# Kernel tuning notes

Hardware: AMD Instinct MI355X
Metric: run time of the kernel (lower is better)

## Reference

```python
import jax, jax.numpy as jnp
import numpy as np

_J6 = jnp.array([[0,0,0,0,0,1],[0,0,0,0,-1,0],[0,0,0,1,0,0],
                 [0,0,1,0,0,0],[0,-1,0,0,0,0],[1,0,0,0,0,0]], dtype=jnp.float32)
_PAIRS4 = [(0,1),(0,2),(0,3),(1,2),(1,3),(2,3)]
H = 16  # n_heads

def _ln(x, g, b, eps=1e-5):
    m = jnp.mean(x, axis=-1, keepdims=True)
    v = jnp.var(x, axis=-1, keepdims=True)
    return (x - m) / jnp.sqrt(v + eps) * g + b

def _exterior(p1, p2):
    # Plucker coordinates of the line through p1,p2 in R^4 -> R^6, normalized
    parts = [p1[..., i] * p2[..., j] - p1[..., j] * p2[..., i] for i, j in _PAIRS4]
    L = jnp.stack(parts, axis=-1)
    n = jnp.linalg.norm(L, axis=-1, keepdims=True)
    return L / jnp.maximum(n, 1e-12)

def _iterated_gram_attn(x, Wqkv, bqkv, W1w, W2w, W1r, W2r, Wmv, bmv, Wmg, bmg,
                        mem_scale, iter_mix, decay_logits, Wout, bout):
    B, T, D = x.shape
    dh = D // H
    # ---- standard causal attention branch ----
    qkv = (x @ Wqkv + bqkv).reshape(B, T, 3, H, dh)
    q = jnp.transpose(qkv[:, :, 0], (0, 2, 1, 3))  # bhtd
    k = jnp.transpose(qkv[:, :, 1], (0, 2, 1, 3))
    v = jnp.transpose(qkv[:, :, 2], (0, 2, 1, 3))
    scores = jnp.einsum('bhtd,bhsd->bhts', q, k) * (dh ** -0.5)
    causal = jnp.tril(jnp.ones((T, T), dtype=bool))
    scores = jnp.where(causal, scores, -jnp.inf)
    attn = jax.nn.softmax(scores, axis=-1)  # dropout is eval-mode identity
    seq_out = jnp.einsum('bhts,bhsd->bhtd', attn, v).transpose(0, 2, 1, 3).reshape(B, T, D)
    # ---- Gram memory branch ----
    x_prev = jnp.concatenate([jnp.zeros_like(x[:, :1]), x[:, :-1]], axis=1)
    w1 = (x_prev @ W1w).reshape(B, T, H, 4)
    w2 = (x @ W2w).reshape(B, T, H, 4)
    write_lines = _exterior(w1, w2)                       # (B,T,H,6)
    r1 = (x @ W1r).reshape(B, T, H, 4)
    r2 = (x @ W2r).reshape(B, T, H, 4)
    read_lines = _exterior(r1, r2)                        # (B,T,H,6)
    Jw = jnp.einsum('bthi,ij->bhtj', write_lines, _J6)    # (B,H,T,6)
    rd = jnp.transpose(read_lines, (0, 2, 1, 3))          # (B,H,T,6)
    decays = jax.nn.sigmoid(decay_logits)                 # (H,)
    pos = jnp.arange(T, dtype=x.dtype)
    outer = Jw[..., :, None] * Jw[..., None, :]           # (B,H,T,6,6)
    dinv = (1.0 / jnp.maximum(decays, 1e-6))[:, None] ** pos[None, :]  # (H,T)
    M = jnp.cumsum(outer * dinv[None, :, :, None, None], axis=2)
    M = jnp.concatenate([jnp.zeros_like(M[:, :, :1]), M[:, :, :-1]], axis=2)  # shift: strictly past
    dfwd = decays[:, None] ** pos[None, :]
    M = M * dfwd[None, :, :, None, None]                  # (B,H,T,6,6)
    rdM = jnp.einsum('bhti,bhtij->bhtj', rd, M)
    score_M = jnp.sum(rdM * rd, axis=-1)                  # (B,H,T)
    score_M2 = jnp.sum(rdM * rdM, axis=-1)
    alpha = jax.nn.sigmoid(iter_mix[0])
    mem_score = (1 - alpha) * score_M + alpha * score_M2
    mem_val = x @ Wmv + bmv                               # (B,T,D)
    gate = jax.nn.sigmoid(x @ Wmg + bmg)                  # (B,T,H)
    gated = jax.nn.sigmoid(jnp.transpose(mem_score, (0, 2, 1)) * mem_scale[None, None, :]) * gate
    gated = jnp.mean(gated, axis=-1, keepdims=True)       # (B,T,1)
    return (seq_out + gated * mem_val) @ Wout + bout

def _block(x, ln1_g, ln1_b, Wqkv, bqkv, W1w, W2w, W1r, W2r, Wmv, bmv, Wmg, bmg,
           mem_scale, iter_mix, decay_logits, Wout, bout,
           ln2_g, ln2_b, Wfc, bfc, Wproj, bproj):
    h = _ln(x, ln1_g, ln1_b)
    x = x + _iterated_gram_attn(h, Wqkv, bqkv, W1w, W2w, W1r, W2r, Wmv, bmv,
                                Wmg, bmg, mem_scale, iter_mix, decay_logits, Wout, bout)
    h2 = _ln(x, ln2_g, ln2_b)
    mlp = jax.nn.gelu(h2 @ Wfc + bfc, approximate=False) @ Wproj + bproj
    return x + mlp

def setup_inputs() -> dict:
    key = jax.random.key(0)
    B, T, D = 2, 1024, 1024
    dff = 4 * D
    ks = jax.random.split(key, 16)
    s = 0.02
    inp = {
        'x': jax.random.normal(ks[0], (B, T, D), jnp.float32),
        'ln1_g': jnp.ones((D,), jnp.float32), 'ln1_b': jnp.zeros((D,), jnp.float32),
        'Wqkv': jax.random.normal(ks[1], (D, 3 * D), jnp.float32) * s,
        'bqkv': jnp.zeros((3 * D,), jnp.float32),
        'W1w': jax.random.normal(ks[2], (D, 4 * H), jnp.float32) * s,
        'W2w': jax.random.normal(ks[3], (D, 4 * H), jnp.float32) * s,
        'W1r': jax.random.normal(ks[4], (D, 4 * H), jnp.float32) * s,
        'W2r': jax.random.normal(ks[5], (D, 4 * H), jnp.float32) * s,
        'Wmv': jax.random.normal(ks[6], (D, D), jnp.float32) * s,
        'bmv': jnp.zeros((D,), jnp.float32),
        'Wmg': jax.random.normal(ks[7], (D, H), jnp.float32) * s,
        'bmg': jnp.zeros((H,), jnp.float32),
        'mem_scale': jnp.full((H,), 0.1, jnp.float32),
        'iter_mix': jnp.zeros((1,), jnp.float32),
        'decay_logits': jnp.full((H,), 4.6, jnp.float32) + 0.1 * jax.random.normal(ks[8], (H,), jnp.float32),
        'Wout': jax.random.normal(ks[9], (D, D), jnp.float32) * s,
        'bout': jnp.zeros((D,), jnp.float32),
        'ln2_g': jnp.ones((D,), jnp.float32), 'ln2_b': jnp.zeros((D,), jnp.float32),
        'Wfc': jax.random.normal(ks[10], (D, dff), jnp.float32) * s,
        'bfc': jnp.zeros((dff,), jnp.float32),
        'Wproj': jax.random.normal(ks[11], (dff, D), jnp.float32) * s,
        'bproj': jnp.zeros((D,), jnp.float32),
    }
    return inp

def reference(x, ln1_g, ln1_b, Wqkv, bqkv, W1w, W2w, W1r, W2r, Wmv, bmv, Wmg, bmg,
              mem_scale, iter_mix, decay_logits, Wout, bout,
              ln2_g, ln2_b, Wfc, bfc, Wproj, bproj):
    return _block(x, ln1_g, ln1_b, Wqkv, bqkv, W1w, W2w, W1r, W2r, Wmv, bmv, Wmg, bmg,
                  mem_scale, iter_mix, decay_logits, Wout, bout,
                  ln2_g, ln2_b, Wfc, bfc, Wproj, bproj)
```

## Files before the change

### kernel.cpp

```cpp
#include <hip/hip_runtime.h>
#include <hip/hip_bf16.h>
#include <math.h>

typedef float f32x4 __attribute__((ext_vector_type(4)));
typedef _Float16 f16x8 __attribute__((ext_vector_type(8)));
typedef _Float16 f16x4 __attribute__((ext_vector_type(4)));

#define TT 1024
#define DD 1024
#define QS 4608

typedef __attribute__((address_space(1))) const void gas_void;
typedef __attribute__((address_space(3))) void las_void;
static __device__ __forceinline__ void gl_lds16(const void* g, void* l) {
  __builtin_amdgcn_global_load_lds((gas_void*)g, (las_void*)l, 16, 0, 0);
}

__global__ __launch_bounds__(256) void gemm_t16(
    const _Float16* __restrict__ A, const _Float16* __restrict__ Wt,
    const float* __restrict__ bias, void* __restrict__ Cv,
    int N, int K, int act, int gx, int mode, int ktiles) {
  __shared__ __align__(16) _Float16 As[2][128 * 32];
  __shared__ __align__(16) _Float16 Bs[2][128 * 32];
  const int tid = threadIdx.x;
  const int lane = tid & 63;
  const int wid = tid >> 6;
  const int wr = wid >> 1, wc = wid & 1;
  const int g = lane >> 4, l16 = lane & 15;
  const int cpx = gridDim.x >> 3;
  const int wg = (blockIdx.x & 7) * cpx + (blockIdx.x >> 3);
  const int row0 = (wg / gx) * 128, col0 = (wg % gx) * 128;
  const int kbeg = blockIdx.y * ktiles * 32;

  f32x4 acc[4][4];
#pragma unroll
  for (int m = 0; m < 4; ++m)
#pragma unroll
    for (int n = 0; n < 4; ++n) acc[m][n] = (f32x4){0.f, 0.f, 0.f, 0.f};

  const int srow = tid >> 2;
  const int goff = ((tid & 3) ^ ((srow >> 1) & 3)) << 3;
  const _Float16* agp = A + (size_t)(row0 + srow) * K + goff;
  const _Float16* bgp = Wt + (size_t)(col0 + srow) * K + goff;
  const size_t half = (size_t)64 * K;
  const int ldst = wid * 64 * 16;

  const int prm = (l16 >> 1) & 3;

#pragma unroll
  for (int i = 0; i < 2; ++i) {
    gl_lds16(agp + i * half + kbeg, (char*)As[0] + i * 4096 + ldst);
    gl_lds16(bgp + i * half + kbeg, (char*)Bs[0] + i * 4096 + ldst);
  }
  __syncthreads();

  int cur = 0;
  for (int kt = 0; kt < ktiles; ++kt) {
    if (kt + 1 < ktiles) {
      const int kp = kbeg + (kt + 1) * 32;
#pragma unroll
      for (int i = 0; i < 2; ++i) {
        gl_lds16(agp + i * half + kp, (char*)As[cur ^ 1] + i * 4096 + ldst);
        gl_lds16(bgp + i * half + kp, (char*)Bs[cur ^ 1] + i * 4096 + ldst);
      }
    }
    f16x8 af[4], bf[4];
#pragma unroll
    for (int m = 0; m < 4; ++m) {
      const int r = wr * 64 + m * 16 + l16;
      af[m] = *(const f16x8*)(As[cur] + r * 32 + ((g ^ prm) << 3));
    }
#pragma unroll
    for (int n = 0; n < 4; ++n) {
      const int r = wc * 64 + n * 16 + l16;
      bf[n] = *(const f16x8*)(Bs[cur] + r * 32 + ((g ^ prm) << 3));
    }
#pragma unroll
    for (int m = 0; m < 4; ++m)
#pragma unroll
      for (int n = 0; n < 4; ++n)
        acc[m][n] = __builtin_amdgcn_mfma_f32_16x16x32_f16(af[m], bf[n], acc[m][n], 0, 0, 0);
    __syncthreads();
    cur ^= 1;
  }
#pragma unroll
  for (int m = 0; m < 4; ++m) {
#pragma unroll
    for (int n = 0; n < 4; ++n) {
      const int col = col0 + wc * 64 + n * 16 + l16;
      const float bv = (mode != 2 && bias) ? bias[col] : 0.f;
#pragma unroll
      for (int rg = 0; rg < 4; ++rg) {
        const int row = row0 + wr * 64 + m * 16 + g * 4 + rg;
        const size_t off = (size_t)row * N + col;
        float v = acc[m][n][rg] + bv;
        if (act == 1) v = 0.5f * v * (1.f + erff(v * 0.70710678118654752f));
        if (mode == 2) atomicAdd(&((float*)Cv)[off], v);
        else ((_Float16*)Cv)[off] = (_Float16)v;
      }
    }
  }
}

__global__ __launch_bounds__(256) void transT(const float* __restrict__ W,
                                              _Float16* __restrict__ WT, int K, int N) {
  __shared__ float tile[64][65];
  const int n0 = blockIdx.x * 64, k0 = blockIdx.y * 64;
  const int tn = threadIdx.x & 63, tk4 = threadIdx.x >> 6;
#pragma unroll
  for (int it = 0; it < 16; ++it) {
    const int k = k0 + it * 4 + tk4;
    tile[tn][it * 4 + tk4] = W[(size_t)k * N + n0 + tn];
  }
  __syncthreads();
  const int on = threadIdx.x >> 2, ok = threadIdx.x & 3;
  f16x8 a, b;
#pragma unroll
  for (int j = 0; j < 8; ++j) {
    a[j] = (_Float16)tile[on][ok * 16 + j];
    b[j] = (_Float16)tile[on][ok * 16 + 8 + j];
  }
  _Float16* dst = WT + (size_t)(n0 + on) * K + k0 + ok * 16;
  *(f16x8*)dst = a;
  *(f16x8*)(dst + 8) = b;
}

__global__ __launch_bounds__(256) void prep_megaT(
    const float* __restrict__ Wqkv, const float* __restrict__ W1w, const float* __restrict__ W2w,
    const float* __restrict__ W1r, const float* __restrict__ W2r, const float* __restrict__ Wmg,
    const float* __restrict__ Wmv, _Float16* __restrict__ WmT) {
  __shared__ float tile[64][65];
  const int n0 = blockIdx.x * 64, k0 = blockIdx.y * 64;
  const int tn = threadIdx.x & 63, tk4 = threadIdx.x >> 6;
#pragma unroll
  for (int it = 0; it < 16; ++it) {
    const int k = k0 + it * 4 + tk4;
    const int n = n0 + tn;
    float v;
    if (n < 3072) v = Wqkv[(size_t)k * 3072 + n];
    else if (n < 3136) v = W1w[k * 64 + n - 3072];
    else if (n < 3200) v = W2w[k * 64 + n - 3136];
    else if (n < 3264) v = W1r[k * 64 + n - 3200];
    else if (n < 3328) v = W2r[k * 64 + n - 3264];
    else if (n < 3344) v = Wmg[k * 16 + n - 3328];
    else if (n < 3584) v = 0.f;
    else v = Wmv[(size_t)k * 1024 + n - 3584];
    tile[tn][it * 4 + tk4] = v;
  }
  __syncthreads();
  const int on = threadIdx.x >> 2, ok = threadIdx.x & 3;
  f16x8 a, b;
#pragma unroll
  for (int j = 0; j < 8; ++j) {
    a[j] = (_Float16)tile[on][ok * 16 + j];
    b[j] = (_Float16)tile[on][ok * 16 + 8 + j];
  }
  _Float16* dst = WmT + (size_t)(n0 + on) * 1024 + k0 + ok * 16;
  *(f16x8*)dst = a;
  *(f16x8*)(dst + 8) = b;
}

__global__ void bm_init(const float* __restrict__ bqkv, const float* __restrict__ bmg,
                        const float* __restrict__ bmv, float* __restrict__ bm) {
  const int col = blockIdx.x * 256 + threadIdx.x;
  if (col >= 4608) return;
  float b = 0.f;
  if (col < 3072) b = bqkv[col];
  else if (col >= 3328 && col < 3344) b = bmg[col - 3328];
  else if (col >= 3584) b = bmv[col - 3584];
  bm[col] = b;
}

__global__ __launch_bounds__(256) void ln16(const float* __restrict__ in,
    const float* __restrict__ gw, const float* __restrict__ bw, _Float16* __restrict__ out) {
  const int row = blockIdx.x, tid = threadIdx.x;
  const float* x = in + (size_t)row * DD;
  const float4 v = *(const float4*)(x + tid * 4);
  float s = v.x + v.y + v.z + v.w;
  float sq = v.x * v.x + v.y * v.y + v.z * v.z + v.w * v.w;
#pragma unroll
  for (int off = 32; off >= 1; off >>= 1) { s += __shfl_xor(s, off); sq += __shfl_xor(sq, off); }
  __shared__ float red[8];
  const int lane = tid & 63, wv = tid >> 6;
  if (lane == 0) { red[wv] = s; red[4 + wv] = sq; }
  __syncthreads();
  s = red[0] + red[1] + red[2] + red[3];
  sq = red[4] + red[5] + red[6] + red[7];
  const float mean = s * (1.f / 1024.f);
  const float var = sq * (1.f / 1024.f) - mean * mean;
  const float rstd = rsqrtf(var + 1e-5f);
  const float4 g4 = *(const float4*)(gw + tid * 4);
  const float4 b4 = *(const float4*)(bw + tid * 4);
  f16x4 o;
  o[0] = (_Float16)((v.x - mean) * rstd * g4.x + b4.x);
  o[1] = (_Float16)((v.y - mean) * rstd * g4.y + b4.y);
  o[2] = (_Float16)((v.z - mean) * rstd * g4.z + b4.z);
  o[3] = (_Float16)((v.w - mean) * rstd * g4.w + b4.w);
  *(f16x4*)(out + (size_t)row * DD + tid * 4) = o;
}

static __device__ __forceinline__ int swzA(int row, int k) {
  return row * 64 + ((((k >> 3) ^ row) & 7) << 3) + (k & 7);
}
static __device__ __forceinline__ int swzV(int row, int k) {
  return row * 64 + ((((k >> 3) ^ row ^ (row >> 3)) & 7) << 3) + (k & 7);
}

__global__ __launch_bounds__(256) void attn_mfma(const _Float16* __restrict__ qkv,
                                                 _Float16* __restrict__ seq_out) {
  __shared__ __align__(16) _Float16 Kl[64 * 64];
  __shared__ __align__(16) _Float16 Vt[64 * 64];
  __shared__ __align__(16) _Float16 Pl[4][16 * 64];
  const int tid = threadIdx.x, lane = tid & 63, wq = tid >> 6;
  const int g = lane >> 4, l16 = lane & 15;
  const int qt = blockIdx.x, hh = blockIdx.y, bb = blockIdx.z;
  const int nt = qt + 1;

  f16x8 qf[2];
  {
    const _Float16* qp = qkv + (size_t)(bb * TT + qt * 64 + wq * 16 + l16) * QS + hh * 64;
#pragma unroll
    for (int ks = 0; ks < 2; ++ks) {
      const f16x8 a = *(const f16x8*)(qp + ks * 32 + g * 8);
#pragma unroll
      for (int j = 0; j < 8; ++j) qf[ks][j] = (_Float16)((float)a[j] * 0.125f);
    }
  }

  f32x4 oacc[4];
#pragma unroll
  for (int n = 0; n < 4; ++n) oacc[n] = (f32x4){0.f, 0.f, 0.f, 0.f};
  float m[4] = {-INFINITY, -INFINITY, -INFINITY, -INFINITY};
  float l[4] = {0.f, 0.f, 0.f, 0.f};

  const int skey = tid >> 2, sc4 = tid & 3;

  for (int tt = 0; tt < nt; ++tt) {
    if (tt) __syncthreads();
    {
      const _Float16* kp = qkv + (size_t)(bb * TT + tt * 64 + skey) * QS + hh * 64 + 1024;
      const _Float16* vp = kp + 1024;
#pragma unroll
      for (int ii = 0; ii < 4; ++ii) {
        const int d0 = sc4 * 4 + ii * 16;
        *(f16x4*)(Kl + swzA(skey, d0)) = *(const f16x4*)(kp + d0);
        const f16x4 vv = *(const f16x4*)(vp + d0);
        Vt[swzV(d0 + 0, skey)] = vv[0];
        Vt[swzV(d0 + 1, skey)] = vv[1];
        Vt[swzV(d0 + 2, skey)] = vv[2];
        Vt[swzV(d0 + 3, skey)] = vv[3];
      }
    }
    __syncthreads();
    f32x4 s[4];
#pragma unroll
    for (int n = 0; n < 4; ++n) s[n] = (f32x4){0.f, 0.f, 0.f, 0.f};
#pragma unroll
    for (int ks = 0; ks < 2; ++ks) {
      f16x8 kf[4];
#pragma unroll
      for (int n = 0; n < 4; ++n) kf[n] = *(const f16x8*)(Kl + swzA(n * 16 + l16, ks * 32 + g * 8));
#pragma unroll
      for (int n = 0; n < 4; ++n)
        s[n] = __builtin_amdgcn_mfma_f32_16x16x32_f16(qf[ks], kf[n], s[n], 0, 0, 0);
    }
    if (tt == qt) {
      const int rloc = wq * 16 + g * 4;
#pragma unroll
      for (int n = 0; n < 4; ++n) {
        const int cloc = n * 16 + l16;
#pragma unroll
        for (int reg = 0; reg < 4; ++reg)
          if (cloc > rloc + reg) s[n][reg] = -INFINITY;
      }
    }
    float f[4];
#pragma unroll
    for (int reg = 0; reg < 4; ++reg) {
      float t = fmaxf(fmaxf(s[0][reg], s[1][reg]), fmaxf(s[2][reg], s[3][reg]));
#pragma unroll
      for (int off = 1; off < 16; off <<= 1) t = fmaxf(t, __shfl_xor(t, off));
      const float nm = fmaxf(m[reg], t);
      f[reg] = __expf(m[reg] - nm);
      m[reg] = nm;
    }
    float rs[4] = {0.f, 0.f, 0.f, 0.f};
#pragma unroll
    for (int n = 0; n < 4; ++n) {
#pragma unroll
      for (int reg = 0; reg < 4; ++reg) {
        const float p = __expf(s[n][reg] - m[reg]);
        rs[reg] += p;
        Pl[wq][swzA(g * 4 + reg, n * 16 + l16)] = (_Float16)p;
      }
    }
#pragma unroll
    for (int reg = 0; reg < 4; ++reg) {
      float t = rs[reg];
#pragma unroll
      for (int off = 1; off < 16; off <<= 1) t += __shfl_xor(t, off);
      l[reg] = l[reg] * f[reg] + t;
    }
#pragma unroll
    for (int n = 0; n < 4; ++n)
#pragma unroll
      for (int reg = 0; reg < 4; ++reg) oacc[n][reg] *= f[reg];
#pragma unroll
    for (int ks = 0; ks < 2; ++ks) {
      const f16x8 pa = *(const f16x8*)(Pl[wq] + swzA(l16, ks * 32 + g * 8));
      f16x8 vb[4];
#pragma unroll
      for (int n = 0; n < 4; ++n) vb[n] = *(const f16x8*)(Vt + swzV(n * 16 + l16, ks * 32 + g * 8));
#pragma unroll
      for (int n = 0; n < 4; ++n)
        oacc[n] = __builtin_amdgcn_mfma_f32_16x16x32_f16(pa, vb[n], oacc[n], 0, 0, 0);
    }
  }
#pragma unroll
  for (int n = 0; n < 4; ++n) {
#pragma unroll
    for (int reg = 0; reg < 4; ++reg) {
      const int r = qt * 64 + wq * 16 + g * 4 + reg;
      seq_out[(size_t)(bb * TT + r) * DD + hh * 64 + n * 16 + l16] = (_Float16)(oacc[n][reg] / l[reg]);
    }
  }
}

static __device__ __forceinline__ void ext6(const float* a, const float* b, float* L) {
  L[0] = a[0] * b[1] - a[1] * b[0];
  L[1] = a[0] * b[2] - a[2] * b[0];
  L[2] = a[0] * b[3] - a[3] * b[0];
  L[3] = a[1] * b[2] - a[2] * b[1];
  L[4] = a[1] * b[3] - a[3] * b[1];
  L[5] = a[2] * b[3] - a[3] * b[2];
  const float n = sqrtf(L[0]*L[0] + L[1]*L[1] + L[2]*L[2] + L[3]*L[3] + L[4]*L[4] + L[5]*L[5]);
  const float s = 1.f / fmaxf(n, 1e-12f);
#pragma unroll
  for (int i = 0; i < 6; ++i) L[i] *= s;
}

__global__ void lines_post(const _Float16* __restrict__ mega, float* __restrict__ jw,
                           float* __restrict__ rdv, float* __restrict__ gate) {
  const int idx = blockIdx.x * 256 + threadIdx.x;
  const int h = idx & 15;
  const int bt = idx >> 4;
  const int t = bt & 1023;
  const int b = bt >> 10;
  const _Float16* row = mega + (size_t)bt * QS + 3072;
  float w1[4] = {0.f, 0.f, 0.f, 0.f}, w2[4], r1[4], r2[4];
  if (t > 0) {
#pragma unroll
    for (int i = 0; i < 4; ++i) w1[i] = (float)row[-QS + h * 4 + i];
  }
#pragma unroll
  for (int i = 0; i < 4; ++i) {
    w2[i] = (float)row[64 + h * 4 + i];
    r1[i] = (float)row[128 + h * 4 + i];
    r2[i] = (float)row[192 + h * 4 + i];
  }
  const float gp = (float)row[256 + h];
  float wl[6], rl[6];
  ext6(w1, w2, wl);
  ext6(r1, r2, rl);
  const size_t o = ((size_t)(b * 16 + h) * 1024 + t) * 6;
  jw[o + 0] =  wl[5]; jw[o + 1] = -wl[4]; jw[o + 2] =  wl[3];
  jw[o + 3] =  wl[2]; jw[o + 4] = -wl[1]; jw[o + 5] =  wl[0];
#pragma unroll
  for (int i = 0; i < 6; ++i) rdv[o + i] = rl[i];
  gate[idx] = 1.f / (1.f + __expf(-gp));
}

static __device__ __forceinline__ int midx(int i, int j) {
  return (i <= j) ? (i * (13 - i)) / 2 + (j - i) : (j * (13 - j)) / 2 + (i - j);
}

__global__ __launch_bounds__(64) void gram_scan(const float* __restrict__ jwv,
    const float* __restrict__ rdv, const float* __restrict__ decay_logits,
    const float* __restrict__ iter_mix, float* __restrict__ mem_score) {
  const int h = blockIdx.x & 15, b = blockIdx.x >> 4;
  const int lane = threadIdx.x;
  const float decay = 1.f / (1.f + __expf(-decay_logits[h]));
  const float alpha = 1.f / (1.f + __expf(-iter_mix[0]));
  __shared__ float sd[64 * 193];
  const size_t base = (size_t)(b * 16 + h) * 1024 * 6;
  for (int it = 0; it < 96; ++it) {
    const int idx = it * 64 + lane;
    const int t = idx / 6, i = idx - 6 * t;
    const int ld = t >> 4, s = t & 15;
    sd[ld * 193 + s * 6 + i] = jwv[base + idx];
    sd[ld * 193 + 96 + s * 6 + i] = rdv[base + idx];
  }
  __syncthreads();
  const float* seg = sd + lane * 193;

  float C[21];
#pragma unroll
  for (int e = 0; e < 21; ++e) C[e] = 0.f;
  for (int s = 0; s < 16; ++s) {
    float J[6], dJ[6];
#pragma unroll
    for (int i = 0; i < 6; ++i) { J[i] = seg[s * 6 + i]; dJ[i] = decay * J[i]; }
#pragma unroll
    for (int i = 0; i < 6; ++i)
#pragma unroll
      for (int j = i; j < 6; ++j)
        C[midx(i, j)] = decay * C[midx(i, j)] + dJ[i] * J[j];
  }
  const float d2 = decay * decay, d4 = d2 * d2, d8 = d4 * d4;
  float fk = d8 * d8;
#pragma unroll
  for (int k = 0; k < 6; ++k) {
    const int off = 1 << k;
#pragma unroll
    for (int e = 0; e < 21; ++e) {
      const float u = __shfl(C[e], lane - off);
      if (lane >= off) C[e] += fk * u;
    }
    fk = fk * fk;
  }
  float M[21];
#pragma unroll
  for (int e = 0; e < 21; ++e) {
    const float u = __shfl(C[e], lane - 1);
    M[e] = (lane >= 1) ? u : 0.f;
  }
  float* msp = mem_score + (size_t)(b * 16 + h) * 1024 + lane * 16;
  for (int s = 0; s < 16; ++s) {
    float J[6], r[6];
#pragma unroll
    for (int i = 0; i < 6; ++i) { J[i] = seg[s * 6 + i]; r[i] = seg[96 + s * 6 + i]; }
    float rdM[6];
#pragma unroll
    for (int i = 0; i < 6; ++i) {
      float a = 0.f;
#pragma unroll
      for (int j = 0; j < 6; ++j) a += M[midx(i, j)] * r[j];
      rdM[i] = a;
    }
    float s1 = 0.f, s2 = 0.f;
#pragma unroll
    for (int i = 0; i < 6; ++i) { s1 += rdM[i] * r[i]; s2 += rdM[i] * rdM[i]; }
    msp[s] = (1.f - alpha) * s1 + alpha * s2;
    float dJ[6];
#pragma unroll
    for (int i = 0; i < 6; ++i) dJ[i] = decay * J[i];
#pragma unroll
    for (int i = 0; i < 6; ++i)
#pragma unroll
      for (int j = i; j < 6; ++j)
        M[midx(i, j)] = decay * M[midx(i, j)] + dJ[i] * J[j];
  }
}

__global__ void gmean_kernel(const float* __restrict__ ms, const float* __restrict__ gate,
    const float* __restrict__ mem_scale, float* __restrict__ gm) {
  const int bt = blockIdx.x * 256 + threadIdx.x;
  const int b = bt >> 10, t = bt & 1023;
  float acc = 0.f;
#pragma unroll
  for (int h = 0; h < 16; ++h) {
    const float sc = ms[(size_t)(b * 16 + h) * 1024 + t];
    const float gt = gate[(size_t)bt * 16 + h];
    acc += (1.f / (1.f + __expf(-sc * mem_scale[h]))) * gt;
  }
  gm[bt] = acc * (1.f / 16.f);
}

__global__ void combine_kernel(const _Float16* __restrict__ seq, const _Float16* __restrict__ mega,
    const float* __restrict__ gm, _Float16* __restrict__ outp) {
  const int i = blockIdx.x * 256 + threadIdx.x;
  const int bt = i >> 8, c4 = i & 255;
  const float g = gm[bt];
  const f16x4 s4 = *(const f16x4*)(seq + (size_t)i * 4);
  const f16x4 m4 = *(const f16x4*)(mega + (size_t)bt * QS + 3584 + c4 * 4);
  f16x4 o;
#pragma unroll
  for (int j = 0; j < 4; ++j) o[j] = (_Float16)((float)s4[j] + g * (float)m4[j]);
  *(f16x4*)(outp + (size_t)i * 4) = o;
}

__global__ void addb_init(const float* __restrict__ src, const float* __restrict__ bias,
                          float* __restrict__ dst) {
  const size_t i = (size_t)blockIdx.x * 256 + threadIdx.x;
  const int c4 = (int)(i & 255);
  const float4 s = ((const float4*)src)[i];
  const float4 b = ((const float4*)bias)[c4];
  float4 o;
  o.x = s.x + b.x; o.y = s.y + b.y; o.z = s.z + b.z; o.w = s.w + b.w;
  ((float4*)dst)[i] = o;
}

extern "C" void kernel_launch(void* const* d_in, const int* in_sizes, int n_in,
                              void* d_out, int out_size, void* d_ws, size_t ws_size,
                              hipStream_t stream) {
  (void)in_sizes; (void)n_in; (void)out_size; (void)ws_size;
  const float* x       = (const float*)d_in[0];
  const float* ln1_g   = (const float*)d_in[1];
  const float* ln1_b   = (const float*)d_in[2];
  const float* Wqkv    = (const float*)d_in[3];
  const float* bqkv    = (const float*)d_in[4];
  const float* W1w     = (const float*)d_in[5];
  const float* W2w     = (const float*)d_in[6];
  const float* W1r     = (const float*)d_in[7];
  const float* W2r     = (const float*)d_in[8];
  const float* Wmv     = (const float*)d_in[9];
  const float* bmv     = (const float*)d_in[10];
  const float* Wmg     = (const float*)d_in[11];
  const float* bmg     = (const float*)d_in[12];
  const float* mscale  = (const float*)d_in[13];
  const float* itermix = (const float*)d_in[14];
  const float* dlogits = (const float*)d_in[15];
  const float* Wout    = (const float*)d_in[16];
  const float* bout    = (const float*)d_in[17];
  const float* ln2_g   = (const float*)d_in[18];
  const float* ln2_b   = (const float*)d_in[19];
  const float* Wfc     = (const float*)d_in[20];
  const float* bfc     = (const float*)d_in[21];
  const float* Wproj   = (const float*)d_in[22];
  const float* bproj   = (const float*)d_in[23];
  float* out = (float*)d_out;
  float* ws = (float*)d_ws;

  const size_t M1 = 1u << 20;
  _Float16* h16    = (_Float16*)ws;
  _Float16* WmT    = (_Float16*)(ws + 1 * M1);
  float*    bm     = ws + 3407872;
  float*    jw     = ws + 3538944;
  float*    rd     = ws + 3538944 + 196608;
  float*    gate   = ws + 3538944 + 393216;
  float*    ms     = ws + 3538944 + 425984;
  float*    gm     = ws + 3538944 + 458752;
  float*    y      = ws + 4 * M1;
  _Float16* mega   = (_Float16*)(ws + 6 * M1);
  _Float16* fc16   = (_Float16*)(ws + 6 * M1);
  _Float16* seq16  = (_Float16*)(ws + 11010048);
  _Float16* WoutT  = (_Float16*)(ws + 12058624);
  _Float16* WfcT   = (_Float16*)(ws + 12 * M1);
  _Float16* WprojT = (_Float16*)(ws + 14 * M1);

  prep_megaT<<<dim3(72, 16), 256, 0, stream>>>(Wqkv, W1w, W2w, W1r, W2r, Wmg, Wmv, WmT);
  bm_init<<<18, 256, 0, stream>>>(bqkv, bmg, bmv, bm);
  transT<<<dim3(16, 16), 256, 0, stream>>>(Wout, WoutT, 1024, 1024);
  transT<<<dim3(64, 16), 256, 0, stream>>>(Wfc, WfcT, 1024, 4096);
  transT<<<dim3(16, 64), 256, 0, stream>>>(Wproj, WprojT, 4096, 1024);

  ln16<<<2048, 256, 0, stream>>>(x, ln1_g, ln1_b, h16);
  gemm_t16<<<576, 256, 0, stream>>>(h16, WmT, bm, mega, 4608, 1024, 0, 36, 1, 32);
  attn_mfma<<<dim3(16, 16, 2), 256, 0, stream>>>(mega, seq16);
  lines_post<<<128, 256, 0, stream>>>(mega, jw, rd, gate);
  gram_scan<<<32, 64, 0, stream>>>(jw, rd, dlogits, itermix, ms);
  gmean_kernel<<<8, 256, 0, stream>>>(ms, gate, mscale, gm);
  combine_kernel<<<2048, 256, 0, stream>>>(seq16, mega, gm, h16);
  addb_init<<<2048, 256, 0, stream>>>(x, bout, y);
  gemm_t16<<<dim3(128, 4), 256, 0, stream>>>(h16, WoutT, nullptr, y, 1024, 1024, 0, 8, 2, 8);
  ln16<<<2048, 256, 0, stream>>>(y, ln2_g, ln2_b, h16);
  gemm_t16<<<512, 256, 0, stream>>>(h16, WfcT, bfc, fc16, 4096, 1024, 1, 32, 1, 32);
  addb_init<<<2048, 256, 0, stream>>>(y, bproj, out);
  gemm_t16<<<dim3(128, 4), 256, 0, stream>>>(fc16, WprojT, nullptr, out, 1024, 4096, 0, 8, 2, 32);
}
```

Measured before the change: 263.0 us.

## Deepen GEMM LDS pipeline to four stages with explicit vmcnt waits

The fp16 MFMA GEMM moves from a double-buffered LDS scheme to a four-buffer ring that prefetches three k-tiles ahead. The full __syncthreads per iteration is replaced by partial s_waitcnt vmcnt waits plus a single s_barrier, so global-to-LDS loads stay in flight across more compute. This aims to hide global memory latency better. In exchange LDS use doubles, which may lower occupancy, and correctness depends on the hand-counted vmcnt values.

```diff
diff --git a/kernel.cpp b/kernel.cpp
--- a/kernel.cpp
+++ b/kernel.cpp
@@ -20,8 +20,8 @@
     const _Float16* __restrict__ A, const _Float16* __restrict__ Wt,
     const float* __restrict__ bias, void* __restrict__ Cv,
     int N, int K, int act, int gx, int mode, int ktiles) {
-  __shared__ __align__(16) _Float16 As[2][128 * 32];
-  __shared__ __align__(16) _Float16 Bs[2][128 * 32];
+  __shared__ __align__(16) _Float16 As[4][128 * 32];
+  __shared__ __align__(16) _Float16 Bs[4][128 * 32];
   const int tid = threadIdx.x;
   const int lane = tid & 63;
   const int wid = tid >> 6;
@@ -48,40 +48,50 @@
   const int prm = (l16 >> 1) & 3;
 
 #pragma unroll
-  for (int i = 0; i < 2; ++i) {
-    gl_lds16(agp + i * half + kbeg, (char*)As[0] + i * 4096 + ldst);
-    gl_lds16(bgp + i * half + kbeg, (char*)Bs[0] + i * 4096 + ldst);
-  }
-  __syncthreads();
-
-  int cur = 0;
+  for (int p = 0; p < 3; ++p) {
+    if (p < ktiles) {
+      const int kp = kbeg + p * 32;
+#pragma unroll
+      for (int i = 0; i < 2; ++i) {
+        gl_lds16(agp + i * half + kp, (char*)As[p] + i * 4096 + ldst);
+        gl_lds16(bgp + i * half + kp, (char*)Bs[p] + i * 4096 + ldst);
+      }
+    }
+  }
+
   for (int kt = 0; kt < ktiles; ++kt) {
-    if (kt + 1 < ktiles) {
-      const int kp = kbeg + (kt + 1) * 32;
+    const int rem = ktiles - 1 - kt;
+    if (rem >= 2)      asm volatile("s_waitcnt vmcnt(8)" ::: "memory");
+    else if (rem == 1) asm volatile("s_waitcnt vmcnt(4)" ::: "memory");
+    else               asm volatile("s_waitcnt vmcnt(0)" ::: "memory");
+    __builtin_amdgcn_s_barrier();
+    __builtin_amdgcn_sched_barrier(0);
+    if (kt + 3 < ktiles) {
+      const int kp = kbeg + (kt + 3) * 32;
+      const int b3 = (kt + 3) & 3;
 #pragma unroll
       for (int i = 0; i < 2; ++i) {
-        gl_lds16(agp + i * half + kp, (char*)As[cur ^ 1] + i * 4096 + ldst);
-        gl_lds16(bgp + i * half + kp, (char*)Bs[cur ^ 1] + i * 4096 + ldst);
+        gl_lds16(agp + i * half + kp, (char*)As[b3] + i * 4096 + ldst);
+        gl_lds16(bgp + i * half + kp, (char*)Bs[b3] + i * 4096 + ldst);
       }
     }
+    const int cb = kt & 3;
     f16x8 af[4], bf[4];
 #pragma unroll
     for (int m = 0; m < 4; ++m) {
       const int r = wr * 64 + m * 16 + l16;
-      af[m] = *(const f16x8*)(As[cur] + r * 32 + ((g ^ prm) << 3));
+      af[m] = *(const f16x8*)(As[cb] + r * 32 + ((g ^ prm) << 3));
     }
 #pragma unroll
     for (int n = 0; n < 4; ++n) {
       const int r = wc * 64 + n * 16 + l16;
-      bf[n] = *(const f16x8*)(Bs[cur] + r * 32 + ((g ^ prm) << 3));
+      bf[n] = *(const f16x8*)(Bs[cb] + r * 32 + ((g ^ prm) << 3));
     }
 #pragma unroll
     for (int m = 0; m < 4; ++m)
 #pragma unroll
       for (int n = 0; n < 4; ++n)
         acc[m][n] = __builtin_amdgcn_mfma_f32_16x16x32_f16(af[m], bf[n], acc[m][n], 0, 0, 0);
-    __syncthreads();
-    cur ^= 1;
   }
 #pragma unroll
   for (int m = 0; m < 4; ++m) {
```

After: 281.7 us. 1.07x slower.
